# Optimization experiments

Hardware: AMD Instinct MI355X
Metric: run time of the kernel (lower is better)

Reference implementation:

```python
import jax, jax.numpy as jnp
import numpy as np

B, MAX_T, S, H, NB, NA = 64, 511, 1024, 4096, 8, 4


def setup_inputs() -> dict:
    key = jax.random.key(0)
    k1, k2, k3, k4, k5 = jax.random.split(key, 5)
    s_i_batch = jax.random.normal(k1, (B, MAX_T + 1, S), dtype=jnp.float32)
    actions_batch = jax.random.randint(k2, (B, MAX_T), 0, NA, dtype=jnp.int32)
    lengths = jax.random.randint(k3, (B,), 0, MAX_T, dtype=jnp.int32)
    W1 = jax.random.normal(k4, (S, H), dtype=jnp.float32) * (1.0 / np.sqrt(S))
    b1 = jnp.zeros((H,), dtype=jnp.float32)
    W2 = jax.random.normal(k5, (H, NB * NA), dtype=jnp.float32) * (1.0 / np.sqrt(H))
    b2 = jnp.zeros((NB * NA,), dtype=jnp.float32)
    return {"s_i_batch": s_i_batch, "actions_batch": actions_batch,
            "lengths": lengths, "W1": W1, "b1": b1, "W2": W2, "b2": b2}


def reference(s_i_batch, actions_batch, lengths, W1, b1, W2, b2):
    Bc, Tp1, _ = s_i_batch.shape
    maxT = Tp1 - 1
    # control_net: MLP -> per-(option, action) log-probs
    h = jax.nn.relu(jnp.einsum('bts,sh->bth', s_i_batch, W1) + b1)
    logits = (jnp.einsum('bth,ha->bta', h, W2) + b2).reshape(Bc, Tp1, NB, NA)
    action_logps = jax.nn.log_softmax(logits, axis=-1)  # (B, T+1, b, 4)
    # option 0, timesteps 0..max_T-1
    lp0 = action_logps[:, :maxT, 0, :]                  # (B, max_T, 4)
    gathered = jnp.take_along_axis(lp0, actions_batch[..., None].astype(jnp.int32), axis=-1)[..., 0]
    mask = (jnp.arange(maxT)[None, :] < lengths[:, None]).astype(lp0.dtype)  # (B, max_T)
    total_logp = jnp.sum(gathered * mask)
    return -total_logp
```

## Files before the change

kernel.cpp:

```cpp
#include <hip/hip_runtime.h>
#include <math.h>

#define B_    64
#define MAXT  511
#define TP1   512
#define S_    1024
#define H_    4096
#define M_TOTAL (B_*TP1)
#define NITER (S_/32)

typedef __attribute__((ext_vector_type(8))) short  short8;
typedef __attribute__((ext_vector_type(4))) float  float4v;

#define ZBUF_BYTES ((size_t)M_TOTAL*4*sizeof(float))
#define OFFS_OFF   0x80000
#define SBF_OFF    0x81000
#define SBF_BYTES  ((size_t)M_TOTAL*S_*2)
#define W1T_OFF    (SBF_OFF + SBF_BYTES)

static __device__ __forceinline__ unsigned short f2bf(float f) {
    unsigned int u = __float_as_uint(f);
    u = u + 0x7fffu + ((u >> 16) & 1u);
    return (unsigned short)(u >> 16);
}

__global__ __launch_bounds__(64) void offsets_kernel(const int* __restrict__ lengths,
                                                     int* __restrict__ offs) {
    int lane = threadIdx.x;
    int v = lengths[lane];
    int x = v;
#pragma unroll
    for (int d = 1; d < 64; d <<= 1) {
        int y = __shfl_up(x, d);
        if (lane >= d) x += y;
    }
    offs[lane] = x - v;
    if (lane == 63) offs[64] = x;
}

__global__ __launch_bounds__(256) void prep_kernel(const float* __restrict__ s,
                                                   const float* __restrict__ W1,
                                                   const int*   __restrict__ lengths,
                                                   const int*   __restrict__ offs,
                                                   unsigned short* __restrict__ Sb,
                                                   unsigned short* __restrict__ W1T) {
    int bid = blockIdx.x;
    if (bid < 16384) {
        int row = 2 * bid + (threadIdx.x >> 7);
        int b = row >> 9, t = row & 511;
        if (t >= lengths[b]) return;
        int crow = offs[b] + t;
        size_t src = (size_t)row  * S_ + (threadIdx.x & 127) * 8;
        size_t dst = (size_t)crow * S_ + (threadIdx.x & 127) * 8;
        float4v f0 = __builtin_nontemporal_load((const float4v*)(s + src));
        float4v f1 = __builtin_nontemporal_load((const float4v*)(s + src + 4));
        short8 o;
        o[0] = (short)f2bf(f0[0]); o[1] = (short)f2bf(f0[1]);
        o[2] = (short)f2bf(f0[2]); o[3] = (short)f2bf(f0[3]);
        o[4] = (short)f2bf(f1[0]); o[5] = (short)f2bf(f1[1]);
        o[6] = (short)f2bf(f1[2]); o[7] = (short)f2bf(f1[3]);
        *(short8*)(Sb + dst) = o;
    } else {
        __shared__ float tile[32][33];
        int tb = bid - 16384;
        int h0 = (tb & 127) * 32;
        int k0 = (tb >> 7) * 32;
        int tx = threadIdx.x & 31, ty = threadIdx.x >> 5;
        for (int r = ty; r < 32; r += 8)
            tile[r][tx] = __builtin_nontemporal_load(&W1[(size_t)(k0 + r) * H_ + h0 + tx]);
        __syncthreads();
        for (int r = ty; r < 32; r += 8)
            W1T[(size_t)(h0 + r) * S_ + k0 + tx] = f2bf(tile[tx][r]);
    }
}

__global__ __launch_bounds__(256, 3) void gemm_fused_kernel(
        const unsigned short* __restrict__ Sb,
        const unsigned short* __restrict__ W1T,
        const float* __restrict__ b1,
        const float* __restrict__ W2,
        const int*   __restrict__ offs,
        float*       __restrict__ zbuf)
{
    int id   = blockIdx.x;
    int xcd  = id & 7;
    int slot = id >> 3;
    int ntile = xcd * 4 + (slot & 3);
    int mtile = slot >> 2;

    int m0 = mtile * 128;
    if (m0 >= offs[64]) return;

    int n0 = ntile * 128;

    __shared__ unsigned short smemA[2 * 128 * 32];
    __shared__ unsigned short smemB[2 * 128 * 32];

    int tid  = threadIdx.x;
    int wid  = tid >> 6;
    int lane = tid & 63;
    int lane15 = lane & 15;
    int quad   = lane >> 4;
    int wave_m = (wid >> 1) * 64;
    int wave_n = (wid & 1) * 64;

    int cA0 = tid, cA1 = tid + 256;
    int mA0 = cA0 >> 2, cp0 = cA0 & 3, q0 = cp0 ^ ((mA0 >> 1) & 3);
    int mA1 = cA1 >> 2, cp1 = cA1 & 3, q1 = cp1 ^ ((mA1 >> 1) & 3);

    const char* gA0 = (const char*)Sb  + (size_t)(m0 + mA0) * (S_*2) + q0 * 16;
    const char* gA1 = (const char*)Sb  + (size_t)(m0 + mA1) * (S_*2) + q1 * 16;
    const char* gB0 = (const char*)W1T + (size_t)(n0 + mA0) * (S_*2) + q0 * 16;
    const char* gB1 = (const char*)W1T + (size_t)(n0 + mA1) * (S_*2) + q1 * 16;
    char* lwA0 = (char*)smemA + cA0 * 16;
    char* lwA1 = (char*)smemA + cA1 * 16;
    char* lwB0 = (char*)smemB + cA0 * 16;
    char* lwB1 = (char*)smemB + cA1 * 16;

    int aOff[4], bOff[4];
#pragma unroll
    for (int s = 0; s < 4; s++) {
        int ml = wave_m + s * 16 + lane15;
        aOff[s] = ml * 32 + (quad ^ ((ml >> 1) & 3)) * 8;
        int nl = wave_n + s * 16 + lane15;
        bOff[s] = nl * 32 + (quad ^ ((nl >> 1) & 3)) * 8;
    }

    float4v acc[4][4] = {};
    short8 sA0[3], sA1[3], sB0[3], sB1[3];

#pragma unroll
    for (int p = 0; p < 3; p++) {
        sA0[p] = *(const short8*)(gA0 + p * 64);
        sA1[p] = *(const short8*)(gA1 + p * 64);
        sB0[p] = *(const short8*)(gB0 + p * 64);
        sB1[p] = *(const short8*)(gB1 + p * 64);
    }
    *(short8*)lwA0 = sA0[0]; *(short8*)lwA1 = sA1[0];
    *(short8*)lwB0 = sB0[0]; *(short8*)lwB1 = sB1[0];

#pragma unroll
    for (int j = 0; j < NITER; j++) {
        __syncthreads();
        if (j + 3 < NITER) {
            sA0[j % 3] = *(const short8*)(gA0 + (j + 3) * 64);
            sA1[j % 3] = *(const short8*)(gA1 + (j + 3) * 64);
            sB0[j % 3] = *(const short8*)(gB0 + (j + 3) * 64);
            sB1[j % 3] = *(const short8*)(gB1 + (j + 3) * 64);
        }
        if (j + 1 < NITER) {
            int nb = ((j + 1) & 1) * 8192;
            *(short8*)(lwA0 + nb) = sA0[(j + 1) % 3];
            *(short8*)(lwA1 + nb) = sA1[(j + 1) % 3];
            *(short8*)(lwB0 + nb) = sB0[(j + 1) % 3];
            *(short8*)(lwB1 + nb) = sB1[(j + 1) % 3];
        }
        const unsigned short* aP = smemA + (j & 1) * 4096;
        const unsigned short* bP = smemB + (j & 1) * 4096;
        short8 af[4], bf[4];
#pragma unroll
        for (int s = 0; s < 4; s++) {
            af[s] = *(const short8*)(aP + aOff[s]);
            bf[s] = *(const short8*)(bP + bOff[s]);
        }
#pragma unroll
        for (int i = 0; i < 4; i++)
#pragma unroll
            for (int jj = 0; jj < 4; jj++)
                acc[i][jj] = __builtin_amdgcn_mfma_f32_16x16x32_bf16(af[i], bf[jj], acc[i][jj], 0, 0, 0);
    }

    float4v w2r[4];
    float   b1v[4];
#pragma unroll
    for (int ns = 0; ns < 4; ns++) {
        int n_g = n0 + wave_n + ns * 16 + lane15;
        w2r[ns] = *(const float4v*)(W2 + (size_t)n_g * 32);
        b1v[ns] = b1[n_g];
    }
#pragma unroll
    for (int ms = 0; ms < 4; ms++) {
        float p[4][4];
#pragma unroll
        for (int r = 0; r < 4; r++)
#pragma unroll
            for (int c = 0; c < 4; c++) p[r][c] = 0.f;
#pragma unroll
        for (int ns = 0; ns < 4; ns++) {
            float4v av = acc[ms][ns];
#pragma unroll
            for (int r = 0; r < 4; r++) {
                float h = av[r] + b1v[ns];
                h = h > 0.f ? h : 0.f;
                p[r][0] += h * w2r[ns][0];
                p[r][1] += h * w2r[ns][1];
                p[r][2] += h * w2r[ns][2];
                p[r][3] += h * w2r[ns][3];
            }
        }
#pragma unroll
        for (int off = 1; off < 16; off <<= 1)
#pragma unroll
            for (int r = 0; r < 4; r++)
#pragma unroll
                for (int c = 0; c < 4; c++)
                    p[r][c] += __shfl_xor(p[r][c], off);
        if (lane15 < 4) {
            int c = lane15;
#pragma unroll
            for (int r = 0; r < 4; r++) {
                int mg = m0 + wave_m + ms * 16 + quad * 4 + r;
                atomicAdd(&zbuf[(size_t)mg * 4 + c], p[r][c]);
            }
        }
    }
}

__global__ __launch_bounds__(128) void reduce_logp_kernel(
        const float* __restrict__ zbuf,
        const int*   __restrict__ actions,
        const int*   __restrict__ lengths,
        const int*   __restrict__ offs,
        const float* __restrict__ b2,
        float*       __restrict__ out)
{
    int b = blockIdx.x;
    int t = blockIdx.y * 128 + threadIdx.x;
    int len = lengths[b];
    float local = 0.f;
    if (t < MAXT && t < len) {
        int row = offs[b] + t;
        float4v z = *(const float4v*)(zbuf + (size_t)row * 4);
        float z0 = z[0] + b2[0], z1 = z[1] + b2[1], z2 = z[2] + b2[2], z3 = z[3] + b2[3];
        float mx = fmaxf(fmaxf(z0, z1), fmaxf(z2, z3));
        float se = expf(z0 - mx) + expf(z1 - mx) + expf(z2 - mx) + expf(z3 - mx);
        int a = actions[b * MAXT + t];
        float za = (a == 0) ? z0 : (a == 1) ? z1 : (a == 2) ? z2 : z3;
        local = (za - mx) - logf(se);
    }
#pragma unroll
    for (int off = 32; off > 0; off >>= 1) local += __shfl_xor(local, off);
    __shared__ float wsum[2];
    if ((threadIdx.x & 63) == 0) wsum[threadIdx.x >> 6] = local;
    __syncthreads();
    if (threadIdx.x == 0) atomicAdd(out, -(wsum[0] + wsum[1]));
}

extern "C" void kernel_launch(void* const* d_in, const int* in_sizes, int n_in,
                              void* d_out, int out_size, void* d_ws, size_t ws_size,
                              hipStream_t stream) {
    const float* s       = (const float*)d_in[0];
    const int*   actions = (const int*)  d_in[1];
    const int*   lengths = (const int*)  d_in[2];
    const float* W1      = (const float*)d_in[3];
    const float* b1      = (const float*)d_in[4];
    const float* W2      = (const float*)d_in[5];
    const float* b2      = (const float*)d_in[6];

    char* ws = (char*)d_ws;
    float*          zbuf = (float*)ws;
    int*            offs = (int*)(ws + OFFS_OFF);
    unsigned short* Sb   = (unsigned short*)(ws + SBF_OFF);
    unsigned short* W1T  = (unsigned short*)(ws + W1T_OFF);

    hipMemsetAsync(ws, 0, ZBUF_BYTES, stream);
    hipMemsetAsync(d_out, 0, sizeof(float), stream);

    offsets_kernel<<<dim3(1), 64, 0, stream>>>(lengths, offs);
    prep_kernel<<<dim3(16384 + 4096), 256, 0, stream>>>(s, W1, lengths, offs, Sb, W1T);
    gemm_fused_kernel<<<dim3(8192), 256, 0, stream>>>(Sb, W1T, b1, W2, offs, zbuf);
    reduce_logp_kernel<<<dim3(B_, 4), 128, 0, stream>>>(zbuf, actions, lengths, offs, b2, (float*)d_out);
}
```

Before: 426.0 us.

## Fuse offsets scan and log-softmax reduction into prep and GEMM kernels

Removes the separate offsets kernel by having each wave recompute the 64-length prefix scan with shuffles in prep and GEMM kernels. Removes the final reduce kernel by having the last-arriving n-tile block per m-tile, detected via an atomic counter, compute the log-softmax gather and accumulate into the output. This saves two kernel launches and their inter-kernel gaps, at the cost of redundant scans per block, a threadfence/atomic handshake, and atomic reads of zbuf.

New measurement: 669.0 us. 1.57x slower.

```diff
diff --git a/kernel.cpp b/kernel.cpp
--- a/kernel.cpp
+++ b/kernel.cpp
@@ -12,8 +12,8 @@
 typedef __attribute__((ext_vector_type(8))) short  short8;
 typedef __attribute__((ext_vector_type(4))) float  float4v;
 
-#define ZBUF_BYTES ((size_t)M_TOTAL*4*sizeof(float))
-#define OFFS_OFF   0x80000
+#define ZSCRATCH_BYTES 0x81000
+#define CNT_OFF    0x80000
 #define SBF_OFF    0x81000
 #define SBF_BYTES  ((size_t)M_TOTAL*S_*2)
 #define W1T_OFF    (SBF_OFF + SBF_BYTES)
@@ -24,32 +24,31 @@
     return (unsigned short)(u >> 16);
 }
 
-__global__ __launch_bounds__(64) void offsets_kernel(const int* __restrict__ lengths,
-                                                     int* __restrict__ offs) {
-    int lane = threadIdx.x;
-    int v = lengths[lane];
+static __device__ __forceinline__ int wave_scan_len(const int* lengths, int lane, int& v) {
+    v = lengths[lane];
     int x = v;
 #pragma unroll
     for (int d = 1; d < 64; d <<= 1) {
         int y = __shfl_up(x, d);
         if (lane >= d) x += y;
     }
-    offs[lane] = x - v;
-    if (lane == 63) offs[64] = x;
+    return x;
 }
 
 __global__ __launch_bounds__(256) void prep_kernel(const float* __restrict__ s,
                                                    const float* __restrict__ W1,
                                                    const int*   __restrict__ lengths,
-                                                   const int*   __restrict__ offs,
                                                    unsigned short* __restrict__ Sb,
                                                    unsigned short* __restrict__ W1T) {
     int bid = blockIdx.x;
     if (bid < 16384) {
+        int lane = threadIdx.x & 63;
+        int lv; int lx = wave_scan_len(lengths, lane, lv);
         int row = 2 * bid + (threadIdx.x >> 7);
         int b = row >> 9, t = row & 511;
-        if (t >= lengths[b]) return;
-        int crow = offs[b] + t;
+        int len_b = __shfl(lv, b);
+        if (t >= len_b) return;
+        int crow = __shfl(lx - lv, b) + t;
         size_t src = (size_t)row  * S_ + (threadIdx.x & 127) * 8;
         size_t dst = (size_t)crow * S_ + (threadIdx.x & 127) * 8;
         float4v f0 = __builtin_nontemporal_load((const float4v*)(s + src));
@@ -79,9 +78,23 @@
         const unsigned short* __restrict__ W1T,
         const float* __restrict__ b1,
         const float* __restrict__ W2,
-        const int*   __restrict__ offs,
-        float*       __restrict__ zbuf)
+        const int*   __restrict__ lengths,
+        const int*   __restrict__ actions,
+        const float* __restrict__ b2,
+        int*         __restrict__ cnt,
+        float*       __restrict__ zbuf,
+        float*       __restrict__ out)
 {
+    __shared__ int   lastflag;
+    __shared__ int   offs_l[64];
+    __shared__ float wsum[4];
+
+    int tid  = threadIdx.x;
+    int lane = tid & 63;
+
+    int lv; int lx = wave_scan_len(lengths, lane, lv);
+    int M_live = __shfl(lx, 63);
+
     int id   = blockIdx.x;
     int xcd  = id & 7;
     int slot = id >> 3;
@@ -89,16 +102,14 @@
     int mtile = slot >> 2;
 
     int m0 = mtile * 128;
-    if (m0 >= offs[64]) return;
+    if (m0 >= M_live) return;
 
     int n0 = ntile * 128;
 
     __shared__ unsigned short smemA[2 * 128 * 32];
     __shared__ unsigned short smemB[2 * 128 * 32];
 
-    int tid  = threadIdx.x;
     int wid  = tid >> 6;
-    int lane = tid & 63;
     int lane15 = lane & 15;
     int quad   = lane >> 4;
     int wave_m = (wid >> 1) * 64;
@@ -214,36 +225,47 @@
             }
         }
     }
-}
-
-__global__ __launch_bounds__(128) void reduce_logp_kernel(
-        const float* __restrict__ zbuf,
-        const int*   __restrict__ actions,
-        const int*   __restrict__ lengths,
-        const int*   __restrict__ offs,
-        const float* __restrict__ b2,
-        float*       __restrict__ out)
-{
-    int b = blockIdx.x;
-    int t = blockIdx.y * 128 + threadIdx.x;
-    int len = lengths[b];
-    float local = 0.f;
-    if (t < MAXT && t < len) {
-        int row = offs[b] + t;
-        float4v z = *(const float4v*)(zbuf + (size_t)row * 4);
-        float z0 = z[0] + b2[0], z1 = z[1] + b2[1], z2 = z[2] + b2[2], z3 = z[3] + b2[3];
-        float mx = fmaxf(fmaxf(z0, z1), fmaxf(z2, z3));
-        float se = expf(z0 - mx) + expf(z1 - mx) + expf(z2 - mx) + expf(z3 - mx);
-        int a = actions[b * MAXT + t];
-        float za = (a == 0) ? z0 : (a == 1) ? z1 : (a == 2) ? z2 : z3;
-        local = (za - mx) - logf(se);
-    }
-#pragma unroll
-    for (int off = 32; off > 0; off >>= 1) local += __shfl_xor(local, off);
-    __shared__ float wsum[2];
-    if ((threadIdx.x & 63) == 0) wsum[threadIdx.x >> 6] = local;
+
     __syncthreads();
-    if (threadIdx.x == 0) atomicAdd(out, -(wsum[0] + wsum[1]));
+    if (tid == 0) {
+        __threadfence();
+        int old = atomicAdd(&cnt[mtile], 1);
+        lastflag = (old == 31);
+    }
+    __syncthreads();
+    if (lastflag) {
+        __threadfence();
+        if (tid < 64) {
+            int v; int x = wave_scan_len(lengths, tid, v);
+            offs_l[tid] = x - v;
+        }
+        __syncthreads();
+        float local = 0.f;
+        int crow = m0 + tid;
+        if (tid < 128 && crow < M_live) {
+            int lo = 0;
+#pragma unroll
+            for (int s = 32; s > 0; s >>= 1) {
+                int mid = lo + s;
+                if (mid < 64 && offs_l[mid] <= crow) lo = mid;
+            }
+            int t = crow - offs_l[lo];
+            float z0 = atomicAdd(&zbuf[(size_t)crow * 4 + 0], 0.f) + b2[0];
+            float z1 = atomicAdd(&zbuf[(size_t)crow * 4 + 1], 0.f) + b2[1];
+            float z2 = atomicAdd(&zbuf[(size_t)crow * 4 + 2], 0.f) + b2[2];
+            float z3 = atomicAdd(&zbuf[(size_t)crow * 4 + 3], 0.f) + b2[3];
+            float mx = fmaxf(fmaxf(z0, z1), fmaxf(z2, z3));
+            float se = expf(z0 - mx) + expf(z1 - mx) + expf(z2 - mx) + expf(z3 - mx);
+            int a = actions[lo * MAXT + t];
+            float za = (a == 0) ? z0 : (a == 1) ? z1 : (a == 2) ? z2 : z3;
+            local = (za - mx) - logf(se);
+        }
+#pragma unroll
+        for (int off = 32; off > 0; off >>= 1) local += __shfl_xor(local, off);
+        if (lane == 0) wsum[wid] = local;
+        __syncthreads();
+        if (tid == 0) atomicAdd(out, -(wsum[0] + wsum[1] + wsum[2] + wsum[3]));
+    }
 }
 
 extern "C" void kernel_launch(void* const* d_in, const int* in_sizes, int n_in,
@@ -259,15 +281,15 @@
 
     char* ws = (char*)d_ws;
     float*          zbuf = (float*)ws;
-    int*            offs = (int*)(ws + OFFS_OFF);
+    int*            cnt  = (int*)(ws + CNT_OFF);
     unsigned short* Sb   = (unsigned short*)(ws + SBF_OFF);
     unsigned short* W1T  = (unsigned short*)(ws + W1T_OFF);
 
-    hipMemsetAsync(ws, 0, ZBUF_BYTES, stream);
+    hipMemsetAsync(ws, 0, ZSCRATCH_BYTES, stream);
     hipMemsetAsync(d_out, 0, sizeof(float), stream);
 
-    offsets_kernel<<<dim3(1), 64, 0, stream>>>(lengths, offs);
-    prep_kernel<<<dim3(16384 + 4096), 256, 0, stream>>>(s, W1, lengths, offs, Sb, W1T);
-    gemm_fused_kernel<<<dim3(8192), 256, 0, stream>>>(Sb, W1T, b1, W2, offs, zbuf);
-    reduce_logp_kernel<<<dim3(B_, 4), 128, 0, stream>>>(zbuf, actions, lengths, offs, b2, (float*)d_out);
-}
+    prep_kernel<<<dim3(16384 + 4096), 256, 0, stream>>>(s, W1, lengths, Sb, W1T);
+    gemm_fused_kernel<<<dim3(8192), 256, 0, stream>>>(Sb, W1T, b1, W2, lengths,
+                                                      actions, b2, cnt, zbuf,
+                                                      (float*)d_out);
+}
```
